# Kernel tuning notes

Hardware: AMD Instinct MI355X
Metric: run time of the kernel (lower is better)

The kernel has to match this reference:

```python
import jax, jax.numpy as jnp
import numpy as np

DEPTH = 5
B, CHANNELS, LENGTH = 256, 10, 128


def setup_inputs() -> dict:
    key = jax.random.key(0)
    # torch module convention: (batch, channels, length); transposed internally to (length, channels)
    path = jax.random.normal(key, (B, CHANNELS, LENGTH), dtype=jnp.float32)
    return {"path": path, "depth": DEPTH}


def _seg_levels(delta, depth):
    # Signature of a single linear segment with increment delta: level k = delta^{\otimes k} / k!
    # delta: (B, d) -> list of (B, d**k) for k = 1..depth
    b = delta.shape[0]
    levels = [delta]
    cur = delta
    for k in range(2, depth + 1):
        cur = (cur[:, :, None] * delta[:, None, :]).reshape(b, -1) / k
        levels.append(cur)
    return levels


def _signature(path_ld, depth):
    # path_ld: (B, L, d) piecewise-linear path; returns (B, sum_k d**k)
    b, L, d = path_ld.shape
    inc = path_ld[:, 1:] - path_ld[:, :-1]  # (B, L-1, d) segment increments
    init = tuple(_seg_levels(inc[:, 0], depth))

    def step(carry, delta):
        # Chen's relation: (S \otimes T)_k = S_k + T_k + sum_{i=1}^{k-1} S_i \otimes T_{k-i}
        T = _seg_levels(delta, depth)
        new = []
        for k in range(1, depth + 1):
            acc = carry[k - 1] + T[k - 1]
            for i in range(1, k):
                acc = acc + (carry[i - 1][:, :, None] * T[k - i - 1][:, None, :]).reshape(b, d ** k)
            new.append(acc)
        return tuple(new), None

    deltas = jnp.swapaxes(inc[:, 1:], 0, 1)  # (L-2, B, d) remaining segments
    final, _ = jax.lax.scan(step, init, deltas)
    return jnp.concatenate(final, axis=-1)


def reference(path, depth):
    # path: (B, channels, length) as in the torch module; iisignature sees (length, channels)
    return _signature(jnp.swapaxes(path, 1, 2), depth)
```

## Files before the change

### kernel.cpp

```cpp
#include <hip/hip_runtime.h>


#define D10    10
#define LPATH  128
#define NSEG   127
#define BLOCK  512
#define NROW   256
#define NROWA  250
#define NCOL   112
#define NCOLA  110
#define KC     16
#define NCH    8
#define SD     132
#define OUT_PER_B 111110

typedef __attribute__((ext_vector_type(8))) short bf16x8;
typedef __attribute__((ext_vector_type(4))) float f32x4;

__device__ __forceinline__ unsigned pack_split(float x, float y, unsigned &lo)
{
    unsigned xb = __float_as_uint(x), yb = __float_as_uint(y);
    float xr = x - __uint_as_float(xb & 0xffff0000u);
    float yr = y - __uint_as_float(yb & 0xffff0000u);
    lo = (__float_as_uint(xr) >> 16) | (__float_as_uint(yr) & 0xffff0000u);
    return (xb >> 16) | (yb & 0xffff0000u);
}

__global__ __launch_bounds__(BLOCK, 2) void sig_kernel(
        const float* __restrict__ path,
        float* __restrict__ out)
{
    __shared__ __align__(16) float dTT[D10 * SD];
    __shared__ __align__(16) float RT [D10 * SD];
    __shared__ __align__(16) short Ahi[4 * NROW * 8];
    __shared__ __align__(16) short Alo[4 * NROW * 8];
    __shared__ __align__(16) short Bhi[4 * NCOL * 8];
    __shared__ __align__(16) short Blo[4 * NCOL * 8];

    const int tid = threadIdx.x;
    const int bb  = blockIdx.x;
    const int b   = bb >> 2;
    const int q   = bb & 3;
    const float* pb = path + (size_t)b * (D10 * LPATH);

    for (int idx = tid; idx < D10 * SD; idx += BLOCK) {
        int c = idx / SD, t = idx - c * SD;
        float d = 0.f, r = 0.f;
        if (t < NSEG) {
            float p1 = pb[c * LPATH + t + 1];
            d = p1 - pb[c * LPATH + t];
            r = pb[c * LPATH + NSEG] - p1;
        }
        dTT[idx] = d;
        RT [idx] = r;
    }
    for (int idx = tid; idx < 4 * (NROW - NROWA) * 8; idx += BLOCK) {
        int kg = idx / ((NROW - NROWA) * 8);
        int rem = idx - kg * ((NROW - NROWA) * 8);
        int o = (kg * NROW + NROWA) * 8 + rem;
        Ahi[o] = 0; Alo[o] = 0;
    }
    if (tid < 4 * 2 * 8) {
        int kg = tid >> 4, rem = tid & 15;
        int o = (kg * NCOL + NCOLA) * 8 + rem;
        Bhi[o] = 0; Blo[o] = 0;
    }

    const int grow = q * NROWA + tid;
    const int g   = grow / 100;
    const int m3  = grow - g * 100;
    const int c2  = m3 / 10;
    const int c3  = m3 - c2 * 10;
    const int goff = g * SD, c2off = c2 * SD, c3off = c3 * SD;

    const int cb  = tid >> 2;
    const int kgB = tid & 3;
    int c4o = 0, ebo = 0;
    if (cb < 100) { int c4 = cb / 10; ebo = (cb - c4 * 10) * SD; c4o = c4 * SD; }
    else          { c4o = (cb - 100) * SD; }

    const int lane = tid & 63;
    const int wv   = tid >> 6;
    const int rl   = lane & 15;
    const int kgl  = lane >> 4;

    float s1 = 0.f, s2 = 0.f, s3 = 0.f;
    f32x4 acc[2][7];
#pragma unroll
    for (int i = 0; i < 2; ++i)
#pragma unroll
        for (int nt = 0; nt < 7; ++nt) acc[i][nt] = f32x4{0.f, 0.f, 0.f, 0.f};

    __syncthreads();

    for (int ch = 0; ch < NCH; ++ch) {
        const int kc0 = ch * KC;
        if (tid < NROWA) {
#pragma unroll
            for (int w0 = 0; w0 < KC; w0 += 4) {
                float4 g4 = *(const float4*)&dTT[goff  + kc0 + w0];
                float4 a4 = *(const float4*)&dTT[c2off + kc0 + w0];
                float4 b4 = *(const float4*)&dTT[c3off + kc0 + w0];
                float ga[4] = {g4.x, g4.y, g4.z, g4.w};
                float aa[4] = {a4.x, a4.y, a4.z, a4.w};
                float ba[4] = {b4.x, b4.y, b4.z, b4.w};
                unsigned hw[4], lw[4];
#pragma unroll
                for (int j = 0; j < 4; ++j) {
                    float dg = ga[j], d2 = aa[j], d3 = ba[j];
                    float u24 = s2 + (s1 + dg * 0.25f)     * d2 * (1.f / 3.f);
                    float u25 = s2 + (s1 + dg * 0.2f)      * d2 * 0.25f;
                    float u23 = s2 + (s1 + dg * (1.f/3.f)) * d2 * 0.5f;
                    float w1v = s3 + u24 * d3 * 0.5f;
                    float w0h = 0.5f * (s3 + u25 * d3 * (1.f / 3.f));
                    s3 += u23 * d3;
                    s2 += (s1 + dg * 0.5f) * d2;
                    s1 += dg;
                    hw[j] = pack_split(w1v, w0h, lw[j]);
                }
                const int ai = ((w0 >> 2) * NROW + tid) * 8;
                *(uint4*)&Ahi[ai] = make_uint4(hw[0], hw[1], hw[2], hw[3]);
                *(uint4*)&Alo[ai] = make_uint4(lw[0], lw[1], lw[2], lw[3]);
            }
        }
        if (tid < 440) {
            const int u0 = kc0 + kgB * 4;
            float4 d4 = *(const float4*)&dTT[c4o + u0];
            float da[4] = {d4.x, d4.y, d4.z, d4.w};
            unsigned hw[4], lw[4];
            if (cb < 100) {
                float4 e4 = *(const float4*)&dTT[ebo + u0];
                float4 r4 = *(const float4*)&RT [ebo + u0];
                float ea[4] = {e4.x, e4.y, e4.z, e4.w};
                float ra[4] = {r4.x, r4.y, r4.z, r4.w};
#pragma unroll
                for (int j = 0; j < 4; ++j)
                    hw[j] = pack_split(da[j] * ra[j], da[j] * ea[j], lw[j]);
            } else {
#pragma unroll
                for (int j = 0; j < 4; ++j)
                    hw[j] = pack_split(da[j], 0.f, lw[j]);
            }
            const int bi = (kgB * NCOL + cb) * 8;
            *(uint4*)&Bhi[bi] = make_uint4(hw[0], hw[1], hw[2], hw[3]);
            *(uint4*)&Blo[bi] = make_uint4(lw[0], lw[1], lw[2], lw[3]);
        }
        __syncthreads();
        {
            bf16x8 bh[7], bl[7];
#pragma unroll
            for (int nt = 0; nt < 7; ++nt) {
                const int bi = (kgl * NCOL + nt * 16 + rl) * 8;
                bh[nt] = *(const bf16x8*)&Bhi[bi];
                bl[nt] = *(const bf16x8*)&Blo[bi];
            }
#pragma unroll
            for (int i = 0; i < 2; ++i) {
                const int ai = (kgl * NROW + wv * 32 + i * 16 + rl) * 8;
                bf16x8 ah = *(const bf16x8*)&Ahi[ai];
                bf16x8 al = *(const bf16x8*)&Alo[ai];
#pragma unroll
                for (int nt = 0; nt < 7; ++nt) {
                    acc[i][nt] = __builtin_amdgcn_mfma_f32_16x16x32_bf16(ah, bh[nt], acc[i][nt], 0, 0, 0);
                    acc[i][nt] = __builtin_amdgcn_mfma_f32_16x16x32_bf16(ah, bl[nt], acc[i][nt], 0, 0, 0);
                    acc[i][nt] = __builtin_amdgcn_mfma_f32_16x16x32_bf16(al, bh[nt], acc[i][nt], 0, 0, 0);
                    acc[i][nt] = __builtin_amdgcn_mfma_f32_16x16x32_bf16(al, bl[nt], acc[i][nt], 0, 0, 0);
                }
            }
        }
        __syncthreads();
    }

    float* ob = out + (size_t)b * OUT_PER_B;
    if (tid < NROWA) {
        ob[110 + grow] = s3;
        if (c3 == 0) ob[10 + g * 10 + c2] = s2;
        if (m3 == 0) ob[g] = s1;
    }
#pragma unroll
    for (int i = 0; i < 2; ++i) {
#pragma unroll
        for (int r = 0; r < 4; ++r) {
            const int prow = wv * 32 + i * 16 + kgl * 4 + r;
            if (prow < NROWA) {
                const int gr = q * NROWA + prow;
#pragma unroll
                for (int nt = 0; nt < 7; ++nt) {
                    const int col = nt * 16 + rl;
                    const float v = acc[i][nt][r];
                    if (col < 100)
                        ob[11110 + (size_t)gr * 100 + col] = v;
                    else if (col < NCOLA)
                        ob[1110 + gr * 10 + (col - 100)] = v;
                }
            }
        }
    }
}

extern "C" void kernel_launch(void* const* d_in, const int* in_sizes, int n_in,
                              void* d_out, int out_size, void* d_ws, size_t ws_size,
                              hipStream_t stream) {
    const float* path = (const float*)d_in[0];
    float* out = (float*)d_out;
    int B = in_sizes[0] / (D10 * LPATH);
    sig_kernel<<<B * 4, BLOCK, 0, stream>>>(path, out);
}
```

Baseline: 204.2 us.

## Double-buffer A/B operand tiles to overlap production with MFMA compute

Doubles the shared-memory A and B staging buffers so the next chunk's operands are computed and packed while the current chunk's MFMAs run. This removes one barrier per chunk. The B-tile work moves from threads 0-439 to threads 256-511, so A-producing and B-producing waves are disjoint. Launch bounds drop from 2 to 1 block per CU, which frees registers but may lower occupancy, and the extra shared memory may also limit residency.

```diff
diff --git a/kernel.cpp b/kernel.cpp
--- a/kernel.cpp
+++ b/kernel.cpp
@@ -26,16 +26,16 @@
     return (xb >> 16) | (yb & 0xffff0000u);
 }
 
-__global__ __launch_bounds__(BLOCK, 2) void sig_kernel(
+__global__ __launch_bounds__(BLOCK, 1) void sig_kernel(
         const float* __restrict__ path,
         float* __restrict__ out)
 {
     __shared__ __align__(16) float dTT[D10 * SD];
     __shared__ __align__(16) float RT [D10 * SD];
-    __shared__ __align__(16) short Ahi[4 * NROW * 8];
-    __shared__ __align__(16) short Alo[4 * NROW * 8];
-    __shared__ __align__(16) short Bhi[4 * NCOL * 8];
-    __shared__ __align__(16) short Blo[4 * NCOL * 8];
+    __shared__ __align__(16) short AhiS[2][4 * NROW * 8];
+    __shared__ __align__(16) short AloS[2][4 * NROW * 8];
+    __shared__ __align__(16) short BhiS[2][4 * NCOL * 8];
+    __shared__ __align__(16) short BloS[2][4 * NCOL * 8];
 
     const int tid = threadIdx.x;
     const int bb  = blockIdx.x;
@@ -54,16 +54,21 @@
         dTT[idx] = d;
         RT [idx] = r;
     }
-    for (int idx = tid; idx < 4 * (NROW - NROWA) * 8; idx += BLOCK) {
-        int kg = idx / ((NROW - NROWA) * 8);
-        int rem = idx - kg * ((NROW - NROWA) * 8);
-        int o = (kg * NROW + NROWA) * 8 + rem;
-        Ahi[o] = 0; Alo[o] = 0;
-    }
-    if (tid < 4 * 2 * 8) {
-        int kg = tid >> 4, rem = tid & 15;
-        int o = (kg * NCOL + NCOLA) * 8 + rem;
-        Bhi[o] = 0; Blo[o] = 0;
+    for (int idx = tid; idx < 2 * 4 * (NROW - NROWA) * 8; idx += BLOCK) {
+        int bufi = idx / (4 * 6 * 8);
+        int rem  = idx - bufi * (4 * 6 * 8);
+        int kg   = rem / (6 * 8);
+        int rr   = rem - kg * (6 * 8);
+        int o = (kg * NROW + NROWA) * 8 + rr;
+        AhiS[bufi][o] = 0; AloS[bufi][o] = 0;
+    }
+    if (tid < 2 * 4 * 2 * 8) {
+        int bufi = tid >> 6;
+        int rem  = tid & 63;
+        int kg   = rem >> 4;
+        int rr   = rem & 15;
+        int o = (kg * NCOL + NCOLA) * 8 + rr;
+        BhiS[bufi][o] = 0; BloS[bufi][o] = 0;
     }
 
     const int grow = q * NROWA + tid;
@@ -73,12 +78,6 @@
     const int c3  = m3 - c2 * 10;
     const int goff = g * SD, c2off = c2 * SD, c3off = c3 * SD;
 
-    const int cb  = tid >> 2;
-    const int kgB = tid & 3;
-    int c4o = 0, ebo = 0;
-    if (cb < 100) { int c4 = cb / 10; ebo = (cb - c4 * 10) * SD; c4o = c4 * SD; }
-    else          { c4o = (cb - 100) * SD; }
-
     const int lane = tid & 63;
     const int wv   = tid >> 6;
     const int rl   = lane & 15;
@@ -91,10 +90,7 @@
 #pragma unroll
         for (int nt = 0; nt < 7; ++nt) acc[i][nt] = f32x4{0.f, 0.f, 0.f, 0.f};
 
-    __syncthreads();
-
-    for (int ch = 0; ch < NCH; ++ch) {
-        const int kc0 = ch * KC;
+    auto produce = [&](int pp, int kc0) {
         if (tid < NROWA) {
 #pragma unroll
             for (int w0 = 0; w0 < KC; w0 += 4) {
@@ -119,55 +115,70 @@
                     hw[j] = pack_split(w1v, w0h, lw[j]);
                 }
                 const int ai = ((w0 >> 2) * NROW + tid) * 8;
-                *(uint4*)&Ahi[ai] = make_uint4(hw[0], hw[1], hw[2], hw[3]);
-                *(uint4*)&Alo[ai] = make_uint4(lw[0], lw[1], lw[2], lw[3]);
-            }
-        }
-        if (tid < 440) {
-            const int u0 = kc0 + kgB * 4;
-            float4 d4 = *(const float4*)&dTT[c4o + u0];
-            float da[4] = {d4.x, d4.y, d4.z, d4.w};
-            unsigned hw[4], lw[4];
-            if (cb < 100) {
-                float4 e4 = *(const float4*)&dTT[ebo + u0];
-                float4 r4 = *(const float4*)&RT [ebo + u0];
-                float ea[4] = {e4.x, e4.y, e4.z, e4.w};
-                float ra[4] = {r4.x, r4.y, r4.z, r4.w};
-#pragma unroll
-                for (int j = 0; j < 4; ++j)
-                    hw[j] = pack_split(da[j] * ra[j], da[j] * ea[j], lw[j]);
-            } else {
-#pragma unroll
-                for (int j = 0; j < 4; ++j)
-                    hw[j] = pack_split(da[j], 0.f, lw[j]);
-            }
-            const int bi = (kgB * NCOL + cb) * 8;
-            *(uint4*)&Bhi[bi] = make_uint4(hw[0], hw[1], hw[2], hw[3]);
-            *(uint4*)&Blo[bi] = make_uint4(lw[0], lw[1], lw[2], lw[3]);
-        }
-        __syncthreads();
-        {
-            bf16x8 bh[7], bl[7];
+                *(uint4*)&AhiS[pp][ai] = make_uint4(hw[0], hw[1], hw[2], hw[3]);
+                *(uint4*)&AloS[pp][ai] = make_uint4(lw[0], lw[1], lw[2], lw[3]);
+            }
+        } else if (tid >= 256) {
+            for (int s = tid - 256; s < 4 * NCOLA; s += 256) {
+                const int cb  = s >> 2;
+                const int kgB = s & 3;
+                int c4o, ebo = 0;
+                if (cb < 100) { int c4 = cb / 10; ebo = (cb - c4 * 10) * SD; c4o = c4 * SD; }
+                else          { c4o = (cb - 100) * SD; }
+                const int u0 = kc0 + kgB * 4;
+                float4 d4 = *(const float4*)&dTT[c4o + u0];
+                float da[4] = {d4.x, d4.y, d4.z, d4.w};
+                unsigned hw[4], lw[4];
+                if (cb < 100) {
+                    float4 e4 = *(const float4*)&dTT[ebo + u0];
+                    float4 r4 = *(const float4*)&RT [ebo + u0];
+                    float ea[4] = {e4.x, e4.y, e4.z, e4.w};
+                    float ra[4] = {r4.x, r4.y, r4.z, r4.w};
+#pragma unroll
+                    for (int j = 0; j < 4; ++j)
+                        hw[j] = pack_split(da[j] * ra[j], da[j] * ea[j], lw[j]);
+                } else {
+#pragma unroll
+                    for (int j = 0; j < 4; ++j)
+                        hw[j] = pack_split(da[j], 0.f, lw[j]);
+                }
+                const int bi = (kgB * NCOL + cb) * 8;
+                *(uint4*)&BhiS[pp][bi] = make_uint4(hw[0], hw[1], hw[2], hw[3]);
+                *(uint4*)&BloS[pp][bi] = make_uint4(lw[0], lw[1], lw[2], lw[3]);
+            }
+        }
+    };
+
+    __syncthreads();
+    produce(0, 0);
+    __syncthreads();
+
+    for (int ch = 0; ch < NCH; ++ch) {
+        const int p = ch & 1;
+        bf16x8 bh[7], bl[7];
+#pragma unroll
+        for (int nt = 0; nt < 7; ++nt) {
+            const int bi = (kgl * NCOL + nt * 16 + rl) * 8;
+            bh[nt] = *(const bf16x8*)&BhiS[p][bi];
+            bl[nt] = *(const bf16x8*)&BloS[p][bi];
+        }
+        bf16x8 ah[2], al[2];
+#pragma unroll
+        for (int i = 0; i < 2; ++i) {
+            const int ai = (kgl * NROW + wv * 32 + i * 16 + rl) * 8;
+            ah[i] = *(const bf16x8*)&AhiS[p][ai];
+            al[i] = *(const bf16x8*)&AloS[p][ai];
+        }
+        if (ch + 1 < NCH) produce(p ^ 1, (ch + 1) * KC);
+#pragma unroll
+        for (int i = 0; i < 2; ++i)
 #pragma unroll
             for (int nt = 0; nt < 7; ++nt) {
-                const int bi = (kgl * NCOL + nt * 16 + rl) * 8;
-                bh[nt] = *(const bf16x8*)&Bhi[bi];
-                bl[nt] = *(const bf16x8*)&Blo[bi];
-            }
-#pragma unroll
-            for (int i = 0; i < 2; ++i) {
-                const int ai = (kgl * NROW + wv * 32 + i * 16 + rl) * 8;
-                bf16x8 ah = *(const bf16x8*)&Ahi[ai];
-                bf16x8 al = *(const bf16x8*)&Alo[ai];
-#pragma unroll
-                for (int nt = 0; nt < 7; ++nt) {
-                    acc[i][nt] = __builtin_amdgcn_mfma_f32_16x16x32_bf16(ah, bh[nt], acc[i][nt], 0, 0, 0);
-                    acc[i][nt] = __builtin_amdgcn_mfma_f32_16x16x32_bf16(ah, bl[nt], acc[i][nt], 0, 0, 0);
-                    acc[i][nt] = __builtin_amdgcn_mfma_f32_16x16x32_bf16(al, bh[nt], acc[i][nt], 0, 0, 0);
-                    acc[i][nt] = __builtin_amdgcn_mfma_f32_16x16x32_bf16(al, bl[nt], acc[i][nt], 0, 0, 0);
-                }
-            }
-        }
+                acc[i][nt] = __builtin_amdgcn_mfma_f32_16x16x32_bf16(ah[i], bh[nt], acc[i][nt], 0, 0, 0);
+                acc[i][nt] = __builtin_amdgcn_mfma_f32_16x16x32_bf16(ah[i], bl[nt], acc[i][nt], 0, 0, 0);
+                acc[i][nt] = __builtin_amdgcn_mfma_f32_16x16x32_bf16(al[i], bh[nt], acc[i][nt], 0, 0, 0);
+                acc[i][nt] = __builtin_amdgcn_mfma_f32_16x16x32_bf16(al[i], bl[nt], acc[i][nt], 0, 0, 0);
+            }
         __syncthreads();
     }
 
```

After: 193.0 us. -5.5%, faster.
